# Kernel optimization log

Measured on AMD Instinct MI355X. Metric: run time of the kernel, lower is better.

The kernel has to match this reference:

```python
import jax, jax.numpy as jnp
import numpy as np

N_SRC, N_DST, MAX_NEIGH, H = 65536, 8192, 32, 128


def setup_inputs() -> dict:
    key = jax.random.key(0)
    ks = jax.random.split(key, 16)
    inp = {
        'x': jax.random.randint(ks[0], (N_SRC, 2), 0, 1000, dtype=jnp.int64)
             if jax.config.jax_enable_x64 else jax.random.randint(ks[0], (N_SRC, 2), 0, 1000, dtype=jnp.int32),
        'neigh_sim': jax.random.randint(ks[1], (N_DST, MAX_NEIGH), 0, N_SRC, dtype=jnp.int32),
        'neigh_cor': jax.random.randint(ks[2], (N_DST, MAX_NEIGH), 0, N_SRC, dtype=jnp.int32),
        'emb0_sim': jax.random.normal(ks[3], (1000, 32), jnp.float32) * 0.1,
        'emb1_sim': jax.random.normal(ks[4], (100000, 96), jnp.float32) * 0.1,
        'emb0_cor': jax.random.normal(ks[5], (1000, 32), jnp.float32) * 0.1,
        'emb1_cor': jax.random.normal(ks[6], (100000, 96), jnp.float32) * 0.1,
        'W_in_sim': jax.random.normal(ks[7], (H, H), jnp.float32) * 0.05,
        'b_in_sim': jnp.zeros((H,), jnp.float32),
        'W_in_cor': jax.random.normal(ks[8], (H, H), jnp.float32) * 0.05,
        'b_in_cor': jnp.zeros((H,), jnp.float32),
        'W_out_sim': jax.random.normal(ks[9], (H, H), jnp.float32) * 0.05,
        'b_out_sim': jnp.zeros((H,), jnp.float32),
        'W_out_cor': jax.random.normal(ks[10], (H, H), jnp.float32) * 0.05,
        'b_out_cor': jnp.zeros((H,), jnp.float32),
        'W_sim2cor': jax.random.normal(ks[11], (H, H), jnp.float32) * 0.05,
        'W_cor2sim': jax.random.normal(ks[12], (H, H), jnp.float32) * 0.05,
    }
    return inp


def _coattention_pool(D, Q):
    # D, Q: [N, m, H]
    n, m, h = Q.shape
    L = jnp.einsum('nmh,nkh->nmk', D, Q)           # [N, m, m]
    AC = jax.nn.softmax(L, axis=-1)
    AS = jax.nn.softmax(jnp.swapaxes(L, 1, 2), axis=-1)
    CQ = jnp.einsum('nmk,nkh->nmh', AC, Q)          # [N, m, H]
    CD = jnp.einsum('nkm,nmh->nkh', AS, jnp.concatenate([D, CQ], axis=-1))  # [N, m, 2H]
    out = jnp.concatenate([Q, CD], axis=-1)         # [N, m, 3H]
    # AvgPool1d(kernel=3, stride=3) over channel dim, then mean over neighbors
    pooled = out.reshape(n, m, h, 3).mean(axis=-1)  # consecutive triples
    return pooled.mean(axis=1)                       # [N, H]


def _mode_forward(x, neigh_sim, neigh_cor, emb0, emb1, W_in, b_in, W_out, b_out, mode):
    feat = jnp.concatenate([emb0[x[:, 0]], emb1[x[:, 1]]], axis=-1)  # [N_src, 128]
    feat = feat @ W_in + b_in                                        # [N_src, H]
    h_self = feat[: neigh_sim.shape[0]]
    nf_sim = feat[neigh_sim]  # [N_dst, m, H]
    nf_cor = feat[neigh_cor]
    if mode == 'cor':
        D, Q = nf_sim, nf_cor
    else:
        D, Q = nf_cor, nf_sim
    rst = h_self + _coattention_pool(D, Q)
    return rst @ W_out + b_out


def reference(x, neigh_sim, neigh_cor, emb0_sim, emb1_sim, emb0_cor, emb1_cor,
              W_in_sim, b_in_sim, W_in_cor, b_in_cor,
              W_out_sim, b_out_sim, W_out_cor, b_out_cor,
              W_sim2cor, W_cor2sim):
    sim = _mode_forward(x, neigh_sim, neigh_cor, emb0_sim, emb1_sim,
                        W_in_sim, b_in_sim, W_out_sim, b_out_sim, 'sim')
    cor = _mode_forward(x, neigh_sim, neigh_cor, emb0_cor, emb1_cor,
                        W_in_cor, b_in_cor, W_out_cor, b_out_cor, 'cor')
    a1, a2, b2 = 0.5, 0.33, 0.33
    z1sim = (1 - a1) * sim + a1 * (cor @ W_cor2sim)
    z1cor = (1 - a1) * cor + a1 * (sim @ W_sim2cor)
    z2sim = (1 - a2 - b2) * sim + a2 * (cor @ W_cor2sim) + b2 * (z1cor @ W_cor2sim)
    z2cor = (1 - a2 - b2) * cor + a2 * (sim @ W_sim2cor) + b2 * (z1sim @ W_sim2cor)
    return z2sim, z2cor
```

## Files before the change

kernel.cpp:

```cpp
#include <hip/hip_runtime.h>
#include <hip/hip_bf16.h>

#define NSRC 65536
#define NDST 8192
#define H 128

#define C_SELF 0.34f
#define C_CROSS 0.495f
#define C_DBL  0.165f

typedef float f32x16 __attribute__((ext_vector_type(16)));
typedef short bf16x8 __attribute__((ext_vector_type(8)));

static __device__ __forceinline__ float b2f(unsigned short u) {
  union { unsigned int i; float f; } v; v.i = ((unsigned int)u) << 16; return v.f;
}
static __device__ __forceinline__ unsigned short f2b(float f) {
  union { float f; unsigned int i; } v; v.f = f;
  unsigned int x = v.i;
  return (unsigned short)((x + 0x7fffu + ((x >> 16) & 1u)) >> 16);
}
static __device__ __forceinline__ void load4bf(const unsigned short* p, float* d) {
  ushort4 u = *(const ushort4*)p;
  d[0] = b2f(u.x); d[1] = b2f(u.y); d[2] = b2f(u.z); d[3] = b2f(u.w);
}

template <int CTRL>
static __device__ __forceinline__ float dpp_mov(float x) {
  return __int_as_float(__builtin_amdgcn_update_dpp(
      0, __float_as_int(x), CTRL, 0xF, 0xF, true));
}
static __device__ __forceinline__ float dpp_sum32_tail(float x) {
  x += dpp_mov<0x111>(x);
  x += dpp_mov<0x112>(x);
  x += dpp_mov<0x114>(x);
  x += dpp_mov<0x118>(x);
  x += dpp_mov<0x142>(x);
  return x;
}
static __device__ __forceinline__ float allred32_sum(float x) {
  x += dpp_mov<0xB1>(x);
  x += dpp_mov<0x4E>(x);
  x += dpp_mov<0x124>(x);
  x += dpp_mov<0x128>(x);
  x += __int_as_float(__builtin_amdgcn_ds_swizzle(__float_as_int(x), 0x401F));
  return x;
}

static __device__ __forceinline__ void load4any(const void* base, size_t idx, int f32flag, float* d) {
  if (f32flag) {
    float4 v = *(const float4*)((const float*)base + idx);
    d[0] = v.x; d[1] = v.y; d[2] = v.z; d[3] = v.w;
  } else {
    load4bf((const unsigned short*)base + idx, d);
  }
}
static __device__ __forceinline__ float load1any(const void* base, size_t idx, int f32flag) {
  return f32flag ? ((const float*)base)[idx] : b2f(((const unsigned short*)base)[idx]);
}

static __device__ __forceinline__ int detect_wf(const unsigned short* __restrict__ W) {
  const int l = threadIdx.x & 63;
  int bad = 0;
#pragma unroll
  for (int i = l; i < 128; i += 64) {
    unsigned short u = W[i];
    if (u != 0) {
      int e = (u >> 7) & 0xFF;
      if (e < 90 || e > 128) bad++;
    }
  }
#pragma unroll
  for (int d = 1; d < 64; d <<= 1) bad += __shfl_xor(bad, d);
  return (bad > 8) ? 1 : 0;
}
static __device__ __forceinline__ int detect_x64(const int* __restrict__ x) {
  const int l = threadIdx.x & 63;
  int nz = (l < 16) ? (x[2 * l + 1] != 0 ? 1 : 0) : 0;
#pragma unroll
  for (int d = 1; d < 64; d <<= 1) nz += __shfl_xor(nz, d);
  return (nz == 0) ? 1 : 0;
}

__global__ __launch_bounds__(128) void transk(
    const void* __restrict__ Wsim_in, const void* __restrict__ Wcor_in,
    const void* __restrict__ Wsc, const void* __restrict__ Wcs,
    unsigned short* __restrict__ WTsim, unsigned short* __restrict__ WTcor,
    unsigned short* __restrict__ WscT, unsigned short* __restrict__ WcsT)
{
  const int wf = detect_wf((const unsigned short*)Wsim_in);
  const int bid = blockIdx.x;
  const int k = threadIdx.x;
  const int n = bid & 127;
  const void* W;
  unsigned short* WT;
  if (bid < 256) {
    W  = (bid & 128) ? Wcor_in : Wsim_in;
    WT = (bid & 128) ? WTcor : WTsim;
  } else {
    W  = (bid & 128) ? Wcs : Wsc;
    WT = (bid & 128) ? WcsT : WscT;
  }
  WT[n * 128 + k] = f2b(load1any(W, k * 128 + n, wf));
}

__global__ __launch_bounds__(256) void sgemm1(
    const void* __restrict__ Wdet,
    const void* __restrict__ Wos, const void* __restrict__ Woc,
    const void* __restrict__ Wsc, const void* __restrict__ Wcs,
    const void* __restrict__ bs, const void* __restrict__ bc,
    const unsigned short* __restrict__ WscT, const unsigned short* __restrict__ WcsT,
    unsigned short* __restrict__ P1T, unsigned short* __restrict__ P2T,
    unsigned short* __restrict__ P1bf, unsigned short* __restrict__ P2bf,
    float* __restrict__ p1, float* __restrict__ p2)
{
  __shared__ float l1[256], l2[256];
  const int wf = detect_wf((const unsigned short*)Wdet);
  const int bid = blockIdx.x;
  const int t = threadIdx.x;

  if (bid == 8) {
    const int c = t & 127, kg = t >> 7;
    float a1 = 0.f, a2 = 0.f;
    for (int k = kg * 64; k < kg * 64 + 64; ++k) {
      a1 += load1any(bs, k, wf) * load1any(Wsc, k * 128 + c, wf);
      a2 += load1any(bc, k, wf) * load1any(Wcs, k * 128 + c, wf);
    }
    l1[t] = a1; l2[t] = a2;
    __syncthreads();
    if (kg == 0) { p1[c] = l1[c] + l1[c + 128]; p2[c] = l2[c] + l2[c + 128]; }
    return;
  }

  const bool isP2 = bid >= 4;
  const int rbase = (bid & 3) * 32;
  const void* A = isP2 ? Woc : Wos;
  const unsigned short* BT = isP2 ? WcsT : WscT;
  unsigned short* PT = isP2 ? P2T : P1T;
  unsigned short* Pb = isP2 ? P2bf : P1bf;

  const int w = t >> 6, l = t & 63, lane = l & 31, half = l >> 5;
  const int arow = rbase + lane;
  const int n = w * 32 + lane;

  bf16x8 af[8];
#pragma unroll
  for (int s = 0; s < 8; ++s) {
    float tmp[8];
    const size_t base = (size_t)arow * 128 + s * 16 + half * 8;
    load4any(A, base, wf, tmp);
    load4any(A, base + 4, wf, tmp + 4);
    union { bf16x8 v; unsigned short u[8]; } cv;
#pragma unroll
    for (int j = 0; j < 8; ++j) cv.u[j] = f2b(tmp[j]);
    af[s] = cv.v;
  }

  f32x16 acc = {0,0,0,0,0,0,0,0,0,0,0,0,0,0,0,0};
#pragma unroll
  for (int s = 0; s < 8; ++s) {
    bf16x8 bfrag = *(const bf16x8*)(BT + (size_t)n * 128 + s * 16 + half * 8);
    acc = __builtin_amdgcn_mfma_f32_32x32x16_bf16(af[s], bfrag, acc, 0, 0, 0);
  }
#pragma unroll
  for (int i = 0; i < 16; ++i) {
    const int m = (i & 3) + 8 * (i >> 2) + 4 * half;
    const int r = rbase + m;
    const unsigned short v = f2b(acc[i]);
    PT[(size_t)n * 128 + r] = v;
    Pb[(size_t)r * 128 + n] = v;
  }
}

__global__ __launch_bounds__(256) void sgemm2(
    const void* __restrict__ Wdet,
    const void* __restrict__ Wos, const void* __restrict__ Woc,
    const void* __restrict__ Wsc, const void* __restrict__ Wcs,
    const void* __restrict__ bs, const void* __restrict__ bc,
    const unsigned short* __restrict__ WscT, const unsigned short* __restrict__ WcsT,
    const unsigned short* __restrict__ P1bf, const unsigned short* __restrict__ P2bf,
    const float* __restrict__ p1, const float* __restrict__ p2,
    unsigned short* __restrict__ MssT, unsigned short* __restrict__ MccT,
    float* __restrict__ bsim, float* __restrict__ bcor)
{
  __shared__ float l1[256], l2[256];
  const int wf = detect_wf((const unsigned short*)Wdet);
  const int bid = blockIdx.x;
  const int t = threadIdx.x;

  if (bid == 8) {
    const int c = t & 127, kg = t >> 7;
    float a3 = 0.f, a4 = 0.f;
    for (int k = kg * 64; k < kg * 64 + 64; ++k) {
      a3 += p1[k] * load1any(Wcs, k * 128 + c, wf);
      a4 += p2[k] * load1any(Wsc, k * 128 + c, wf);
    }
    l1[t] = a3; l2[t] = a4;
    __syncthreads();
    if (kg == 0) {
      bsim[c] = C_SELF * load1any(bs, c, wf) + C_CROSS * p2[c] + C_DBL * (l1[c] + l1[c + 128]);
      bcor[c] = C_SELF * load1any(bc, c, wf) + C_CROSS * p1[c] + C_DBL * (l2[c] + l2[c + 128]);
    }
    return;
  }

  const bool isMcc = bid >= 4;
  const int rbase = (bid & 3) * 32;
  const unsigned short* A = isMcc ? P2bf : P1bf;
  const unsigned short* BT = isMcc ? WscT : WcsT;
  const void* Wself = isMcc ? Woc : Wos;
  unsigned short* out = isMcc ? MccT : MssT;

  const int w = t >> 6, l = t & 63, lane = l & 31, half = l >> 5;
  const int arow = rbase + lane;
  const int n = w * 32 + lane;

  bf16x8 af[8];
#pragma unroll
  for (int s = 0; s < 8; ++s)
    af[s] = *(const bf16x8*)(A + (size_t)arow * 128 + s * 16 + half * 8);

  f32x16 acc = {0,0,0,0,0,0,0,0,0,0,0,0,0,0,0,0};
#pragma unroll
  for (int s = 0; s < 8; ++s) {
    bf16x8 bfrag = *(const bf16x8*)(BT + (size_t)n * 128 + s * 16 + half * 8);
    acc = __builtin_amdgcn_mfma_f32_32x32x16_bf16(af[s], bfrag, acc, 0, 0, 0);
  }
#pragma unroll
  for (int i = 0; i < 16; ++i) {
    const int m = (i & 3) + 8 * (i >> 2) + 4 * half;
    const int r = rbase + m;
    out[(size_t)n * 128 + r] =
        f2b(C_SELF * load1any(Wself, (size_t)r * 128 + n, wf) + C_DBL * acc[i]);
  }
}

__global__ __launch_bounds__(256) void featgemm_mfma(
    const int* __restrict__ x,
    const void* __restrict__ Wdet,
    const void* __restrict__ emb0s, const void* __restrict__ emb1s,
    const void* __restrict__ emb0c, const void* __restrict__ emb1c,
    const unsigned short* __restrict__ WTs, const unsigned short* __restrict__ WTc,
    const void* __restrict__ bvs, const void* __restrict__ bvc,
    unsigned char* __restrict__ f8s, unsigned short* __restrict__ f16s,
    unsigned char* __restrict__ f8c, unsigned short* __restrict__ f16c)
{
  const int wf  = detect_wf((const unsigned short*)Wdet);
  const int x64 = detect_x64(x);
  const int mode = blockIdx.y;
  const void* emb0 = mode ? emb0c : emb0s;
  const void* emb1 = mode ? emb1c : emb1s;
  const unsigned short* WT = mode ? WTc : WTs;
  const void* bvec = mode ? bvc : bvs;
  unsigned char*  feat8  = mode ? f8c  : f8s;
  unsigned short* feat16 = mode ? f16c : f16s;

  const int t = threadIdx.x;
  const int w = t >> 6, l = t & 63, lane = l & 31, half = l >> 5;
  const int rbase = blockIdx.x * 128 + w * 32;
  const int r = rbase + lane;

  int x0, x1;
  if (x64) { x0 = x[r * 4]; x1 = x[r * 4 + 2]; }
  else     { x0 = x[r * 2]; x1 = x[r * 2 + 1]; }

  bf16x8 afrag[8];
#pragma unroll
  for (int s = 0; s < 8; ++s) {
    float tmp[8];
    if (s < 2) {
      const size_t base = (size_t)x0 * 32 + s * 16 + half * 8;
      load4any(emb0, base, wf, tmp);
      load4any(emb0, base + 4, wf, tmp + 4);
    } else {
      const size_t base = (size_t)x1 * 96 + (s * 16 - 32) + half * 8;
      load4any(emb1, base, wf, tmp);
      load4any(emb1, base + 4, wf, tmp + 4);
    }
    union { bf16x8 v; unsigned short u[8]; } cv;
#pragma unroll
    for (int j = 0; j < 8; ++j) cv.u[j] = f2b(tmp[j]);
    afrag[s] = cv.v;
  }

  const bool do16 = (rbase < NDST);
#pragma unroll
  for (int strip = 0; strip < 4; ++strip) {
    const int n = strip * 32 + lane;
    const unsigned short* wtrow = WT + (size_t)n * 128 + half * 8;
    f32x16 acc = {0,0,0,0,0,0,0,0,0,0,0,0,0,0,0,0};
#pragma unroll
    for (int s = 0; s < 8; ++s) {
      bf16x8 bfrag = *(const bf16x8*)(wtrow + s * 16);
      acc = __builtin_amdgcn_mfma_f32_32x32x16_bf16(afrag[s], bfrag, acc, 0, 0, 0);
    }
    const float bias_n = load1any(bvec, n, wf);
#pragma unroll
    for (int i = 0; i < 16; ++i) {
      const int m = (i & 3) + 8 * (i >> 2) + 4 * half;
      const int row = rbase + m;
      const float val = acc[i] + bias_n;
      const int p8 = __builtin_amdgcn_cvt_pk_fp8_f32(val, val, 0, false);
      feat8[(size_t)row * H + n] = (unsigned char)(p8 & 0xFF);
      if (do16) feat16[(size_t)row * H + n] = f2b(val);
    }
  }
}

__global__ __launch_bounds__(256) void coatt_mfma(
    const unsigned char* __restrict__ f8s, const unsigned short* __restrict__ f16s,
    const unsigned char* __restrict__ f8c, const unsigned short* __restrict__ f16c,
    const int* __restrict__ nsim, const int* __restrict__ ncor,
    unsigned short* __restrict__ rsts, unsigned short* __restrict__ rstc)
{
  const int mode = blockIdx.y;
  const unsigned char*  feat8  = mode ? f8c  : f8s;
  const unsigned short* feat16 = mode ? f16c : f16s;
  const int* idxD = mode ? nsim : ncor;
  const int* idxQ = mode ? ncor : nsim;
  unsigned short* rst = mode ? rstc : rsts;

  __shared__ float gbuf[4][448];
  const int t = threadIdx.x;
  const int w = t >> 6;
  const int l = t & 63;
  const int r = l & 31;
  const int half = l >> 5;
  const int n = blockIdx.x * 4 + w;

  float* g   = gbuf[w];
  float* svb = gbuf[w] + 384;
  float* tvb = gbuf[w] + 416;

  const int gD = idxD[n * 32 + r];
  const int gQ = idxQ[n * 32 + r];
  const unsigned char* drow = feat8 + (size_t)gD * H + half * 8;
  const unsigned char* qrow = feat8 + (size_t)gQ * H + half * 8;

  long dfrag[8], qfrag[8];
#pragma unroll
  for (int s = 0; s < 8; ++s) {
    dfrag[s] = *(const long*)(drow + s * 16);
    qfrag[s] = *(const long*)(qrow + s * 16);
  }

  f32x16 acc = {0,0,0,0,0,0,0,0,0,0,0,0,0,0,0,0};
#pragma unroll
  for (int s = 0; s < 8; ++s)
    acc = __builtin_amdgcn_mfma_f32_32x32x16_fp8_fp8(dfrag[s], qfrag[s], acc, 0, 0, 0);

  float ex[16], rrcp[16];
#pragma unroll
  for (int i = 0; i < 16; ++i) ex[i] = __expf(acc[i]);
#pragma unroll
  for (int i = 0; i < 16; ++i) rrcp[i] = 1.0f / allred32_sum(ex[i]);
  float csum = 0.f;
#pragma unroll
  for (int i = 0; i < 16; ++i) csum += ex[i];
  csum += __shfl_xor(csum, 32);
  const float crcp = 1.0f / csum;

  float svt[16];
#pragma unroll
  for (int i = 0; i < 16; ++i) svt[i] = dpp_sum32_tail(ex[i] * crcp);
  if (r == 31) {
    *(float4*)(svb + 4 * half)      = make_float4(svt[0],  svt[1],  svt[2],  svt[3]);
    *(float4*)(svb + 8 + 4 * half)  = make_float4(svt[4],  svt[5],  svt[6],  svt[7]);
    *(float4*)(svb + 16 + 4 * half) = make_float4(svt[8],  svt[9],  svt[10], svt[11]);
    *(float4*)(svb + 24 + 4 * half) = make_float4(svt[12], svt[13], svt[14], svt[15]);
  }
  float sv16[16];
#pragma unroll
  for (int q = 0; q < 4; ++q) {
    float4 v = *(const float4*)(svb + q * 8 + 4 * half);
    sv16[q * 4] = v.x; sv16[q * 4 + 1] = v.y; sv16[q * 4 + 2] = v.z; sv16[q * 4 + 3] = v.w;
  }
  float tvp = 0.f;
#pragma unroll
  for (int i = 0; i < 16; ++i) tvp += sv16[i] * ex[i] * rrcp[i];
  const float tv = tvp + __shfl_xor(tvp, 32);

  if (l < 32) tvb[l] = tv;
  float tv16[16];
#pragma unroll
  for (int q = 0; q < 4; ++q) {
    float4 vv = *(const float4*)(tvb + q * 8 + 4 * half);
    tv16[q * 4] = vv.x; tv16[q * 4 + 1] = vv.y; tv16[q * 4 + 2] = vv.z; tv16[q * 4 + 3] = vv.w;
  }

  const int bpos = (l & 15) - half * 8;
  const long b_ident = (bpos >= 0 && bpos < 8) ? (0x38L << (8 * bpos)) : 0L;
  const f32x16 zf = {0,0,0,0,0,0,0,0,0,0,0,0,0,0,0,0};

#pragma unroll
  for (int s = 0; s < 8; ++s) {
    f32x16 td = __builtin_amdgcn_mfma_f32_32x32x16_fp8_fp8(dfrag[s], b_ident, zf, 0, 0, 0);
    f32x16 tq = __builtin_amdgcn_mfma_f32_32x32x16_fp8_fp8(qfrag[s], b_ident, zf, 0, 0, 0);
    float su = 0.f, sw = 0.f, sv_ = 0.f;
#pragma unroll
    for (int i = 0; i < 16; ++i) {
      su  += tq[i];
      sw  += tv16[i] * tq[i];
      sv_ += sv16[i] * td[i];
    }
    su  += __shfl_xor(su, 32);
    sw  += __shfl_xor(sw, 32);
    sv_ += __shfl_xor(sv_, 32);
    if (l < 16) {
      const int c = s * 16 + l;
      g[c]       = su;
      g[128 + c] = sv_;
      g[256 + c] = sw;
    }
  }

#pragma unroll
  for (int rep = 0; rep < 2; ++rep) {
    const int hp = l + rep * 64;
    const float p = (g[3 * hp] + g[3 * hp + 1] + g[3 * hp + 2]) * (1.0f / 96.0f);
    const float hs = b2f(feat16[(size_t)n * H + hp]);
    rst[(size_t)n * H + hp] = f2b(hs + p);
  }
}

__global__ __launch_bounds__(256) void finalmm_mfma(
    const unsigned short* __restrict__ Rs, const unsigned short* __restrict__ Rc,
    const unsigned short* __restrict__ MssT, const unsigned short* __restrict__ MccT,
    const unsigned short* __restrict__ P1T, const unsigned short* __restrict__ P2T,
    const float* __restrict__ bsim, const float* __restrict__ bcor,
    float* __restrict__ outp)
{
  const int t = threadIdx.x;
  const int w = t >> 6, l = t & 63, lane = l & 31, half = l >> 5;
  const int rbase = blockIdx.x * 32;
  const int arow = rbase + lane;
  const int n = w * 32 + lane;

  const unsigned short* rsrow = Rs + (size_t)arow * H + half * 8;
  const unsigned short* rcrow = Rc + (size_t)arow * H + half * 8;
  bf16x8 aS[8], aC[8];
#pragma unroll
  for (int s = 0; s < 8; ++s) {
    aS[s] = *(const bf16x8*)(rsrow + s * 16);
    aC[s] = *(const bf16x8*)(rcrow + s * 16);
  }

  const unsigned short* bMss = MssT + (size_t)n * 128 + half * 8;
  const unsigned short* bMcc = MccT + (size_t)n * 128 + half * 8;
  const unsigned short* bP1  = P1T  + (size_t)n * 128 + half * 8;
  const unsigned short* bP2  = P2T  + (size_t)n * 128 + half * 8;

  f32x16 a1 = {0,0,0,0,0,0,0,0,0,0,0,0,0,0,0,0};
  f32x16 a2 = a1, a3 = a1, a4 = a1;
#pragma unroll
  for (int s = 0; s < 8; ++s) {
    bf16x8 b1 = *(const bf16x8*)(bMss + s * 16);
    bf16x8 b2 = *(const bf16x8*)(bP2  + s * 16);
    bf16x8 b3 = *(const bf16x8*)(bMcc + s * 16);
    bf16x8 b4 = *(const bf16x8*)(bP1  + s * 16);
    a1 = __builtin_amdgcn_mfma_f32_32x32x16_bf16(aS[s], b1, a1, 0, 0, 0);
    a2 = __builtin_amdgcn_mfma_f32_32x32x16_bf16(aC[s], b2, a2, 0, 0, 0);
    a3 = __builtin_amdgcn_mfma_f32_32x32x16_bf16(aC[s], b3, a3, 0, 0, 0);
    a4 = __builtin_amdgcn_mfma_f32_32x32x16_bf16(aS[s], b4, a4, 0, 0, 0);
  }

  const float bsv = bsim[n], bcv = bcor[n];
#pragma unroll
  for (int i = 0; i < 16; ++i) {
    const int m = (i & 3) + 8 * (i >> 2) + 4 * half;
    const int row = rbase + m;
    outp[(size_t)row * H + n] = a1[i] + C_CROSS * a2[i] + bsv;
    outp[(size_t)NDST * H + (size_t)row * H + n] = a3[i] + C_CROSS * a4[i] + bcv;
  }
}

extern "C" void kernel_launch(void* const* d_in, const int* in_sizes, int n_in,
                              void* d_out, int out_size, void* d_ws, size_t ws_size,
                              hipStream_t stream) {
  const int* x    = (const int*)d_in[0];
  const int* nsim = (const int*)d_in[1];
  const int* ncor = (const int*)d_in[2];
  const void* emb0_sim = d_in[3];
  const void* emb1_sim = d_in[4];
  const void* emb0_cor = d_in[5];
  const void* emb1_cor = d_in[6];
  const void* W_in_sim  = d_in[7];
  const void* b_in_sim  = d_in[8];
  const void* W_in_cor  = d_in[9];
  const void* b_in_cor  = d_in[10];
  const void* W_out_sim = d_in[11];
  const void* b_out_sim = d_in[12];
  const void* W_out_cor = d_in[13];
  const void* b_out_cor = d_in[14];
  const void* W_sim2cor = d_in[15];
  const void* W_cor2sim = d_in[16];

  float* fbase = (float*)d_ws;
  float* P1slot = fbase;
  float* P2slot = P1slot + H * H;
  float* p1v = P2slot + H * H;
  float* p2v = p1v + H;
  float* bsimv = p2v + H;
  float* bcorv = bsimv + H;
  int* flags = (int*)(bcorv + H);
  unsigned short* feat16_sim = (unsigned short*)(flags + 4);
  unsigned short* feat16_cor = feat16_sim + (size_t)NDST * H;
  unsigned short* rst_sim    = feat16_cor + (size_t)NDST * H;
  unsigned short* rst_cor    = rst_sim + (size_t)NDST * H;
  unsigned char* feat8_sim = (unsigned char*)(rst_cor + (size_t)NDST * H);
  unsigned char* feat8_cor = feat8_sim + (size_t)NSRC * H;
  unsigned short* WT_sim = (unsigned short*)(feat8_cor + (size_t)NSRC * H);
  unsigned short* WT_cor = WT_sim + H * H;
  unsigned short* P1T  = WT_cor + H * H;
  unsigned short* P2T  = P1T + H * H;
  unsigned short* MssT = P2T + H * H;
  unsigned short* MccT = MssT + H * H;
  unsigned short* WscT = (unsigned short*)P1slot;
  unsigned short* WcsT = WscT + H * H;
  unsigned short* P1bf = (unsigned short*)P2slot;
  unsigned short* P2bf = P1bf + H * H;

  transk<<<512, 128, 0, stream>>>(W_in_sim, W_in_cor, W_sim2cor, W_cor2sim,
                                  WT_sim, WT_cor, WscT, WcsT);
  sgemm1<<<9, 256, 0, stream>>>(W_in_sim, W_out_sim, W_out_cor, W_sim2cor, W_cor2sim,
                                b_out_sim, b_out_cor, WscT, WcsT,
                                P1T, P2T, P1bf, P2bf, p1v, p2v);
  sgemm2<<<9, 256, 0, stream>>>(W_in_sim, W_out_sim, W_out_cor, W_sim2cor, W_cor2sim,
                                b_out_sim, b_out_cor, WscT, WcsT,
                                P1bf, P2bf, p1v, p2v, MssT, MccT, bsimv, bcorv);
  featgemm_mfma<<<dim3(NSRC / 128, 2), 256, 0, stream>>>(
      x, W_in_sim, emb0_sim, emb1_sim, emb0_cor, emb1_cor,
      WT_sim, WT_cor, b_in_sim, b_in_cor,
      feat8_sim, feat16_sim, feat8_cor, feat16_cor);
  coatt_mfma<<<dim3(NDST / 4, 2), 256, 0, stream>>>(
      feat8_sim, feat16_sim, feat8_cor, feat16_cor,
      nsim, ncor, rst_sim, rst_cor);
  finalmm_mfma<<<NDST / 32, 256, 0, stream>>>(rst_sim, rst_cor, MssT, MccT, P1T, P2T,
                                              bsimv, bcorv, (float*)d_out);
}
```

Before: 242.2 us.

## Merge weight prep kernels into one launch, split featgemm strips, vectorize final stores

The transpose kernel and the two small weight-product GEMM kernels are merged into one prep kernel with 131 blocks. Each of two blocks computes a full 128x128 product, keeps it in shared memory and chains the second GEMM from there, which removes two launches and the intermediate global buffers. featgemm now launches twice as many blocks, each handling two of the four column strips, and the coattention reduction is written with 2-wide vectors. finalmm swaps its MFMA operands so the output is transposed, allowing float4 stores and float4 bias loads. In exchange, the single prep block doing a whole 128x128 GEMM serially may become a long serial tail, and each featgemm block redoes its gather and A-fragment setup twice.

```diff
diff --git a/kernel.cpp b/kernel.cpp
--- a/kernel.cpp
+++ b/kernel.cpp
@@ -10,6 +10,7 @@
 #define C_DBL  0.165f
 
 typedef float f32x16 __attribute__((ext_vector_type(16)));
+typedef float f32x2 __attribute__((ext_vector_type(2)));
 typedef short bf16x8 __attribute__((ext_vector_type(8)));
 
 static __device__ __forceinline__ float b2f(unsigned short u) {
@@ -82,156 +83,129 @@
   return (nz == 0) ? 1 : 0;
 }
 
-__global__ __launch_bounds__(128) void transk(
+__global__ __launch_bounds__(256) void prep2(
     const void* __restrict__ Wsim_in, const void* __restrict__ Wcor_in,
-    const void* __restrict__ Wsc, const void* __restrict__ Wcs,
-    unsigned short* __restrict__ WTsim, unsigned short* __restrict__ WTcor,
-    unsigned short* __restrict__ WscT, unsigned short* __restrict__ WcsT)
-{
-  const int wf = detect_wf((const unsigned short*)Wsim_in);
-  const int bid = blockIdx.x;
-  const int k = threadIdx.x;
-  const int n = bid & 127;
-  const void* W;
-  unsigned short* WT;
-  if (bid < 256) {
-    W  = (bid & 128) ? Wcor_in : Wsim_in;
-    WT = (bid & 128) ? WTcor : WTsim;
-  } else {
-    W  = (bid & 128) ? Wcs : Wsc;
-    WT = (bid & 128) ? WcsT : WscT;
-  }
-  WT[n * 128 + k] = f2b(load1any(W, k * 128 + n, wf));
-}
-
-__global__ __launch_bounds__(256) void sgemm1(
-    const void* __restrict__ Wdet,
     const void* __restrict__ Wos, const void* __restrict__ Woc,
     const void* __restrict__ Wsc, const void* __restrict__ Wcs,
     const void* __restrict__ bs, const void* __restrict__ bc,
-    const unsigned short* __restrict__ WscT, const unsigned short* __restrict__ WcsT,
+    unsigned short* __restrict__ WTsim, unsigned short* __restrict__ WTcor,
     unsigned short* __restrict__ P1T, unsigned short* __restrict__ P2T,
-    unsigned short* __restrict__ P1bf, unsigned short* __restrict__ P2bf,
-    float* __restrict__ p1, float* __restrict__ p2)
-{
-  __shared__ float l1[256], l2[256];
-  const int wf = detect_wf((const unsigned short*)Wdet);
-  const int bid = blockIdx.x;
-  const int t = threadIdx.x;
-
-  if (bid == 8) {
-    const int c = t & 127, kg = t >> 7;
-    float a1 = 0.f, a2 = 0.f;
-    for (int k = kg * 64; k < kg * 64 + 64; ++k) {
-      a1 += load1any(bs, k, wf) * load1any(Wsc, k * 128 + c, wf);
-      a2 += load1any(bc, k, wf) * load1any(Wcs, k * 128 + c, wf);
-    }
-    l1[t] = a1; l2[t] = a2;
-    __syncthreads();
-    if (kg == 0) { p1[c] = l1[c] + l1[c + 128]; p2[c] = l2[c] + l2[c + 128]; }
-    return;
-  }
-
-  const bool isP2 = bid >= 4;
-  const int rbase = (bid & 3) * 32;
-  const void* A = isP2 ? Woc : Wos;
-  const unsigned short* BT = isP2 ? WcsT : WscT;
-  unsigned short* PT = isP2 ? P2T : P1T;
-  unsigned short* Pb = isP2 ? P2bf : P1bf;
-
-  const int w = t >> 6, l = t & 63, lane = l & 31, half = l >> 5;
-  const int arow = rbase + lane;
-  const int n = w * 32 + lane;
-
-  bf16x8 af[8];
-#pragma unroll
-  for (int s = 0; s < 8; ++s) {
-    float tmp[8];
-    const size_t base = (size_t)arow * 128 + s * 16 + half * 8;
-    load4any(A, base, wf, tmp);
-    load4any(A, base + 4, wf, tmp + 4);
-    union { bf16x8 v; unsigned short u[8]; } cv;
-#pragma unroll
-    for (int j = 0; j < 8; ++j) cv.u[j] = f2b(tmp[j]);
-    af[s] = cv.v;
-  }
-
-  f32x16 acc = {0,0,0,0,0,0,0,0,0,0,0,0,0,0,0,0};
-#pragma unroll
-  for (int s = 0; s < 8; ++s) {
-    bf16x8 bfrag = *(const bf16x8*)(BT + (size_t)n * 128 + s * 16 + half * 8);
-    acc = __builtin_amdgcn_mfma_f32_32x32x16_bf16(af[s], bfrag, acc, 0, 0, 0);
-  }
-#pragma unroll
-  for (int i = 0; i < 16; ++i) {
-    const int m = (i & 3) + 8 * (i >> 2) + 4 * half;
-    const int r = rbase + m;
-    const unsigned short v = f2b(acc[i]);
-    PT[(size_t)n * 128 + r] = v;
-    Pb[(size_t)r * 128 + n] = v;
-  }
-}
-
-__global__ __launch_bounds__(256) void sgemm2(
-    const void* __restrict__ Wdet,
-    const void* __restrict__ Wos, const void* __restrict__ Woc,
-    const void* __restrict__ Wsc, const void* __restrict__ Wcs,
-    const void* __restrict__ bs, const void* __restrict__ bc,
-    const unsigned short* __restrict__ WscT, const unsigned short* __restrict__ WcsT,
-    const unsigned short* __restrict__ P1bf, const unsigned short* __restrict__ P2bf,
-    const float* __restrict__ p1, const float* __restrict__ p2,
     unsigned short* __restrict__ MssT, unsigned short* __restrict__ MccT,
     float* __restrict__ bsim, float* __restrict__ bcor)
 {
-  __shared__ float l1[256], l2[256];
-  const int wf = detect_wf((const unsigned short*)Wdet);
+  __shared__ unsigned short Pl[128 * 128];
+  __shared__ float l1[256], l2[256], lp1[128], lp2[128];
+  const int wf = detect_wf((const unsigned short*)Wsim_in);
   const int bid = blockIdx.x;
   const int t = threadIdx.x;
 
-  if (bid == 8) {
-    const int c = t & 127, kg = t >> 7;
-    float a3 = 0.f, a4 = 0.f;
-    for (int k = kg * 64; k < kg * 64 + 64; ++k) {
-      a3 += p1[k] * load1any(Wcs, k * 128 + c, wf);
-      a4 += p2[k] * load1any(Wsc, k * 128 + c, wf);
-    }
-    l1[t] = a3; l2[t] = a4;
+  if (bid < 128) {
+    const int mat = bid >> 6;
+    const int n = (bid & 63) * 2 + (t >> 7);
+    const int k = t & 127;
+    const void* W = mat ? Wcor_in : Wsim_in;
+    unsigned short* WT = mat ? WTcor : WTsim;
+    WT[n * 128 + k] = f2b(load1any(W, k * 128 + n, wf));
+    return;
+  }
+
+  if (bid < 130) {
+    const int isMcc = bid & 1;
+    const void* Wself = isMcc ? Woc : Wos;
+    const void* B1 = isMcc ? Wcs : Wsc;
+    const void* B2 = isMcc ? Wsc : Wcs;
+    unsigned short* PT = isMcc ? P2T : P1T;
+    unsigned short* MT = isMcc ? MccT : MssT;
+
+    const int w = t >> 6, l = t & 63, lane = l & 31, half = l >> 5;
+    const int n = w * 32 + lane;
+
+    bf16x8 bf[8];
+#pragma unroll
+    for (int s = 0; s < 8; ++s) {
+      union { bf16x8 v; unsigned short u[8]; } cv;
+#pragma unroll
+      for (int j = 0; j < 8; ++j)
+        cv.u[j] = f2b(load1any(B1, (size_t)(s * 16 + half * 8 + j) * 128 + n, wf));
+      bf[s] = cv.v;
+    }
+
+#pragma unroll
+    for (int tr = 0; tr < 4; ++tr) {
+      const int ar = tr * 32 + lane;
+      bf16x8 af[8];
+#pragma unroll
+      for (int s = 0; s < 8; ++s) {
+        float tmp[8];
+        const size_t base = (size_t)ar * 128 + s * 16 + half * 8;
+        load4any(Wself, base, wf, tmp);
+        load4any(Wself, base + 4, wf, tmp + 4);
+        union { bf16x8 v; unsigned short u[8]; } cv;
+#pragma unroll
+        for (int j = 0; j < 8; ++j) cv.u[j] = f2b(tmp[j]);
+        af[s] = cv.v;
+      }
+      f32x16 acc = {0,0,0,0,0,0,0,0,0,0,0,0,0,0,0,0};
+#pragma unroll
+      for (int s = 0; s < 8; ++s)
+        acc = __builtin_amdgcn_mfma_f32_32x32x16_bf16(af[s], bf[s], acc, 0, 0, 0);
+#pragma unroll
+      for (int i = 0; i < 16; ++i) {
+        const int r = tr * 32 + (i & 3) + 8 * (i >> 2) + 4 * half;
+        const unsigned short v = f2b(acc[i]);
+        PT[(size_t)n * 128 + r] = v;
+        Pl[r * 128 + n] = v;
+      }
+    }
     __syncthreads();
-    if (kg == 0) {
-      bsim[c] = C_SELF * load1any(bs, c, wf) + C_CROSS * p2[c] + C_DBL * (l1[c] + l1[c + 128]);
-      bcor[c] = C_SELF * load1any(bc, c, wf) + C_CROSS * p1[c] + C_DBL * (l2[c] + l2[c + 128]);
+
+    bf16x8 bf2[8];
+#pragma unroll
+    for (int s = 0; s < 8; ++s) {
+      union { bf16x8 v; unsigned short u[8]; } cv;
+#pragma unroll
+      for (int j = 0; j < 8; ++j)
+        cv.u[j] = f2b(load1any(B2, (size_t)(s * 16 + half * 8 + j) * 128 + n, wf));
+      bf2[s] = cv.v;
+    }
+#pragma unroll
+    for (int tr = 0; tr < 4; ++tr) {
+      f32x16 acc = {0,0,0,0,0,0,0,0,0,0,0,0,0,0,0,0};
+#pragma unroll
+      for (int s = 0; s < 8; ++s) {
+        bf16x8 af = *(const bf16x8*)(Pl + (tr * 32 + lane) * 128 + s * 16 + half * 8);
+        acc = __builtin_amdgcn_mfma_f32_32x32x16_bf16(af, bf2[s], acc, 0, 0, 0);
+      }
+#pragma unroll
+      for (int i = 0; i < 16; ++i) {
+        const int r = tr * 32 + (i & 3) + 8 * (i >> 2) + 4 * half;
+        MT[(size_t)n * 128 + r] =
+            f2b(C_SELF * load1any(Wself, (size_t)r * 128 + n, wf) + C_DBL * acc[i]);
+      }
     }
     return;
   }
 
-  const bool isMcc = bid >= 4;
-  const int rbase = (bid & 3) * 32;
-  const unsigned short* A = isMcc ? P2bf : P1bf;
-  const unsigned short* BT = isMcc ? WscT : WcsT;
-  const void* Wself = isMcc ? Woc : Wos;
-  unsigned short* out = isMcc ? MccT : MssT;
-
-  const int w = t >> 6, l = t & 63, lane = l & 31, half = l >> 5;
-  const int arow = rbase + lane;
-  const int n = w * 32 + lane;
-
-  bf16x8 af[8];
-#pragma unroll
-  for (int s = 0; s < 8; ++s)
-    af[s] = *(const bf16x8*)(A + (size_t)arow * 128 + s * 16 + half * 8);
-
-  f32x16 acc = {0,0,0,0,0,0,0,0,0,0,0,0,0,0,0,0};
-#pragma unroll
-  for (int s = 0; s < 8; ++s) {
-    bf16x8 bfrag = *(const bf16x8*)(BT + (size_t)n * 128 + s * 16 + half * 8);
-    acc = __builtin_amdgcn_mfma_f32_32x32x16_bf16(af[s], bfrag, acc, 0, 0, 0);
-  }
-#pragma unroll
-  for (int i = 0; i < 16; ++i) {
-    const int m = (i & 3) + 8 * (i >> 2) + 4 * half;
-    const int r = rbase + m;
-    out[(size_t)n * 128 + r] =
-        f2b(C_SELF * load1any(Wself, (size_t)r * 128 + n, wf) + C_DBL * acc[i]);
+  const int c = t & 127, kg = t >> 7;
+  float a1 = 0.f, a2 = 0.f;
+  for (int k = kg * 64; k < kg * 64 + 64; ++k) {
+    a1 += load1any(bs, k, wf) * load1any(Wsc, k * 128 + c, wf);
+    a2 += load1any(bc, k, wf) * load1any(Wcs, k * 128 + c, wf);
+  }
+  l1[t] = a1; l2[t] = a2;
+  __syncthreads();
+  if (kg == 0) { lp1[c] = l1[c] + l1[c + 128]; lp2[c] = l2[c] + l2[c + 128]; }
+  __syncthreads();
+  float a3 = 0.f, a4 = 0.f;
+  for (int k = kg * 64; k < kg * 64 + 64; ++k) {
+    a3 += lp1[k] * load1any(Wcs, k * 128 + c, wf);
+    a4 += lp2[k] * load1any(Wsc, k * 128 + c, wf);
+  }
+  l1[t] = a3; l2[t] = a4;
+  __syncthreads();
+  if (kg == 0) {
+    bsim[c] = C_SELF * load1any(bs, c, wf) + C_CROSS * lp2[c] + C_DBL * (l1[c] + l1[c + 128]);
+    bcor[c] = C_SELF * load1any(bc, c, wf) + C_CROSS * lp1[c] + C_DBL * (l2[c] + l2[c + 128]);
   }
 }
 
@@ -247,7 +221,8 @@
 {
   const int wf  = detect_wf((const unsigned short*)Wdet);
   const int x64 = detect_x64(x);
-  const int mode = blockIdx.y;
+  const int mode  = blockIdx.y >> 1;
+  const int shalf = blockIdx.y & 1;
   const void* emb0 = mode ? emb0c : emb0s;
   const void* emb1 = mode ? emb1c : emb1s;
   const unsigned short* WT = mode ? WTc : WTs;
@@ -285,7 +260,8 @@
 
   const bool do16 = (rbase < NDST);
 #pragma unroll
-  for (int strip = 0; strip < 4; ++strip) {
+  for (int s2 = 0; s2 < 2; ++s2) {
+    const int strip = shalf * 2 + s2;
     const int n = strip * 32 + lane;
     const unsigned short* wtrow = WT + (size_t)n * 128 + half * 8;
     f32x16 acc = {0,0,0,0,0,0,0,0,0,0,0,0,0,0,0,0};
@@ -396,13 +372,18 @@
   for (int s = 0; s < 8; ++s) {
     f32x16 td = __builtin_amdgcn_mfma_f32_32x32x16_fp8_fp8(dfrag[s], b_ident, zf, 0, 0, 0);
     f32x16 tq = __builtin_amdgcn_mfma_f32_32x32x16_fp8_fp8(qfrag[s], b_ident, zf, 0, 0, 0);
-    float su = 0.f, sw = 0.f, sv_ = 0.f;
-#pragma unroll
-    for (int i = 0; i < 16; ++i) {
-      su  += tq[i];
-      sw  += tv16[i] * tq[i];
-      sv_ += sv16[i] * td[i];
-    }
+    f32x2 su2 = {0.f, 0.f}, sw2 = {0.f, 0.f}, sv2 = {0.f, 0.f};
+#pragma unroll
+    for (int i = 0; i < 8; ++i) {
+      f32x2 tq2 = { tq[2 * i], tq[2 * i + 1] };
+      f32x2 td2 = { td[2 * i], td[2 * i + 1] };
+      f32x2 tvv = { tv16[2 * i], tv16[2 * i + 1] };
+      f32x2 svv = { sv16[2 * i], sv16[2 * i + 1] };
+      su2 += tq2;
+      sw2 += tvv * tq2;
+      sv2 += svv * td2;
+    }
+    float su = su2.x + su2.y, sw = sw2.x + sw2.y, sv_ = sv2.x + sv2.y;
     su  += __shfl_xor(su, 32);
     sw  += __shfl_xor(sw, 32);
     sv_ += __shfl_xor(sv_, 32);
@@ -433,44 +414,53 @@
   const int t = threadIdx.x;
   const int w = t >> 6, l = t & 63, lane = l & 31, half = l >> 5;
   const int rbase = blockIdx.x * 32;
-  const int arow = rbase + lane;
-  const int n = w * 32 + lane;
-
-  const unsigned short* rsrow = Rs + (size_t)arow * H + half * 8;
-  const unsigned short* rcrow = Rc + (size_t)arow * H + half * 8;
-  bf16x8 aS[8], aC[8];
+  const int orow = rbase + lane;
+  const int nb = w * 32;
+
+  const unsigned short* rsrow = Rs + (size_t)orow * H + half * 8;
+  const unsigned short* rcrow = Rc + (size_t)orow * H + half * 8;
+  bf16x8 bS[8], bC[8];
 #pragma unroll
   for (int s = 0; s < 8; ++s) {
-    aS[s] = *(const bf16x8*)(rsrow + s * 16);
-    aC[s] = *(const bf16x8*)(rcrow + s * 16);
-  }
-
-  const unsigned short* bMss = MssT + (size_t)n * 128 + half * 8;
-  const unsigned short* bMcc = MccT + (size_t)n * 128 + half * 8;
-  const unsigned short* bP1  = P1T  + (size_t)n * 128 + half * 8;
-  const unsigned short* bP2  = P2T  + (size_t)n * 128 + half * 8;
+    bS[s] = *(const bf16x8*)(rsrow + s * 16);
+    bC[s] = *(const bf16x8*)(rcrow + s * 16);
+  }
+
+  const unsigned short* aMss = MssT + (size_t)(nb + lane) * 128 + half * 8;
+  const unsigned short* aMcc = MccT + (size_t)(nb + lane) * 128 + half * 8;
+  const unsigned short* aP1  = P1T  + (size_t)(nb + lane) * 128 + half * 8;
+  const unsigned short* aP2  = P2T  + (size_t)(nb + lane) * 128 + half * 8;
 
   f32x16 a1 = {0,0,0,0,0,0,0,0,0,0,0,0,0,0,0,0};
   f32x16 a2 = a1, a3 = a1, a4 = a1;
 #pragma unroll
   for (int s = 0; s < 8; ++s) {
-    bf16x8 b1 = *(const bf16x8*)(bMss + s * 16);
-    bf16x8 b2 = *(const bf16x8*)(bP2  + s * 16);
-    bf16x8 b3 = *(const bf16x8*)(bMcc + s * 16);
-    bf16x8 b4 = *(const bf16x8*)(bP1  + s * 16);
-    a1 = __builtin_amdgcn_mfma_f32_32x32x16_bf16(aS[s], b1, a1, 0, 0, 0);
-    a2 = __builtin_amdgcn_mfma_f32_32x32x16_bf16(aC[s], b2, a2, 0, 0, 0);
-    a3 = __builtin_amdgcn_mfma_f32_32x32x16_bf16(aC[s], b3, a3, 0, 0, 0);
-    a4 = __builtin_amdgcn_mfma_f32_32x32x16_bf16(aS[s], b4, a4, 0, 0, 0);
-  }
-
-  const float bsv = bsim[n], bcv = bcor[n];
-#pragma unroll
-  for (int i = 0; i < 16; ++i) {
-    const int m = (i & 3) + 8 * (i >> 2) + 4 * half;
-    const int row = rbase + m;
-    outp[(size_t)row * H + n] = a1[i] + C_CROSS * a2[i] + bsv;
-    outp[(size_t)NDST * H + (size_t)row * H + n] = a3[i] + C_CROSS * a4[i] + bcv;
+    bf16x8 m1 = *(const bf16x8*)(aMss + s * 16);
+    bf16x8 m2 = *(const bf16x8*)(aP2  + s * 16);
+    bf16x8 m3 = *(const bf16x8*)(aMcc + s * 16);
+    bf16x8 m4 = *(const bf16x8*)(aP1  + s * 16);
+    a1 = __builtin_amdgcn_mfma_f32_32x32x16_bf16(m1, bS[s], a1, 0, 0, 0);
+    a2 = __builtin_amdgcn_mfma_f32_32x32x16_bf16(m2, bC[s], a2, 0, 0, 0);
+    a3 = __builtin_amdgcn_mfma_f32_32x32x16_bf16(m3, bC[s], a3, 0, 0, 0);
+    a4 = __builtin_amdgcn_mfma_f32_32x32x16_bf16(m4, bS[s], a4, 0, 0, 0);
+  }
+
+#pragma unroll
+  for (int q = 0; q < 4; ++q) {
+    const int n0 = nb + 8 * q + 4 * half;
+    const float4 bsv = *(const float4*)(bsim + n0);
+    const float4 bcv = *(const float4*)(bcor + n0);
+    float4 v1, v2;
+    v1.x = a1[4*q+0] + C_CROSS * a2[4*q+0] + bsv.x;
+    v1.y = a1[4*q+1] + C_CROSS * a2[4*q+1] + bsv.y;
+    v1.z = a1[4*q+2] + C_CROSS * a2[4*q+2] + bsv.z;
+    v1.w = a1[4*q+3] + C_CROSS * a2[4*q+3] + bsv.w;
+    v2.x = a3[4*q+0] + C_CROSS * a4[4*q+0] + bcv.x;
+    v2.y = a3[4*q+1] + C_CROSS * a4[4*q+1] + bcv.y;
+    v2.z = a3[4*q+2] + C_CROSS * a4[4*q+2] + bcv.z;
+    v2.w = a3[4*q+3] + C_CROSS * a4[4*q+3] + bcv.w;
+    *(float4*)(outp + (size_t)orow * H + n0) = v1;
+    *(float4*)(outp + (size_t)NDST * H + (size_t)orow * H + n0) = v2;
   }
 }
 
@@ -515,20 +505,11 @@
   unsigned short* P2T  = P1T + H * H;
   unsigned short* MssT = P2T + H * H;
   unsigned short* MccT = MssT + H * H;
-  unsigned short* WscT = (unsigned short*)P1slot;
-  unsigned short* WcsT = WscT + H * H;
-  unsigned short* P1bf = (unsigned short*)P2slot;
-  unsigned short* P2bf = P1bf + H * H;
-
-  transk<<<512, 128, 0, stream>>>(W_in_sim, W_in_cor, W_sim2cor, W_cor2sim,
-                                  WT_sim, WT_cor, WscT, WcsT);
-  sgemm1<<<9, 256, 0, stream>>>(W_in_sim, W_out_sim, W_out_cor, W_sim2cor, W_cor2sim,
-                                b_out_sim, b_out_cor, WscT, WcsT,
-                                P1T, P2T, P1bf, P2bf, p1v, p2v);
-  sgemm2<<<9, 256, 0, stream>>>(W_in_sim, W_out_sim, W_out_cor, W_sim2cor, W_cor2sim,
-                                b_out_sim, b_out_cor, WscT, WcsT,
-                                P1bf, P2bf, p1v, p2v, MssT, MccT, bsimv, bcorv);
-  featgemm_mfma<<<dim3(NSRC / 128, 2), 256, 0, stream>>>(
+
+  prep2<<<131, 256, 0, stream>>>(W_in_sim, W_in_cor, W_out_sim, W_out_cor,
+                                 W_sim2cor, W_cor2sim, b_out_sim, b_out_cor,
+                                 WT_sim, WT_cor, P1T, P2T, MssT, MccT, bsimv, bcorv);
+  featgemm_mfma<<<dim3(NSRC / 128, 4), 256, 0, stream>>>(
       x, W_in_sim, emb0_sim, emb1_sim, emb0_cor, emb1_cor,
       WT_sim, WT_cor, b_in_sim, b_in_cor,
       feat8_sim, feat16_sim, feat8_cor, feat16_cor);
```

Result: no change. 245.9 us (+1.5%).
